# Kernel tuning notes

Hardware: AMD Instinct MI355X
Metric: run time of the kernel (lower is better)

Reference implementation:

```python
import jax, jax.numpy as jnp
import numpy as np

B, C, L, H = 4, 1024, 2048, 16
D = C // H


def setup_inputs() -> dict:
    key = jax.random.key(0)
    k1, k2, k3, k4 = jax.random.split(key, 4)
    queries = jax.random.normal(k1, (B, C, L), dtype=jnp.float32)
    mask = jax.random.randint(k2, (B, L), 0, 2, dtype=jnp.int32)
    # Conv1d(kernel_size=1, bias=False) weights, stored as [out_ch, in_ch]
    Wm = jax.random.normal(k3, (2 * C, C), dtype=jnp.float32) * (1.0 / np.sqrt(C))
    Wq = jax.random.normal(k4, (C, C), dtype=jnp.float32) * (1.0 / np.sqrt(C))
    return {"queries": queries, "mask": mask, "Wm": Wm, "Wq": Wq}


def reference(queries, mask, Wm, Wq):
    # 1x1 conv == channel-wise linear: [B,C,L] -> [B,L,out]
    mem = jnp.einsum("oc,bcl->blo", Wm, queries)   # [B, L, 2C]
    q = jnp.einsum("oc,bcl->blo", Wq, queries)      # [B, L, C]

    def split_heads(x):  # [B, L, C'] -> [B, H, L, D']
        b, l, c = x.shape
        return x.reshape(b, l, H, c // H).transpose(0, 2, 1, 3)

    Q = split_heads(q) * (D ** -0.5)                # [B, H, L, D]
    K = split_heads(mem[..., :C])                   # [B, H, L, D]
    V = split_heads(mem[..., C:])                   # [B, H, L, D]

    logits = jnp.einsum("bhqd,bhkd->bhqk", Q, K)    # [B, H, L, L]
    m = mask.astype(jnp.float32)[:, None, None, :]  # [B, 1, 1, L]
    NEG_INF = jnp.float32(-1e30)
    logits = logits * m + (1.0 - m) * NEG_INF
    weights = jax.nn.softmax(logits, axis=-1)
    x = jnp.einsum("bhqk,bhkd->bhqd", weights, V)   # [B, H, L, D]
    # combine heads and return [B, C, L]
    out = x.transpose(0, 2, 1, 3).reshape(B, L, C).transpose(0, 2, 1)
    return out
```

## Files before the change

kernel.cpp:

```cpp
#include <hip/hip_runtime.h>


typedef __bf16 bf16x8 __attribute__((ext_vector_type(8)));
typedef float f32x4 __attribute__((ext_vector_type(4)));
typedef float f32x16 __attribute__((ext_vector_type(16)));
typedef unsigned int u32x4 __attribute__((ext_vector_type(4)));

#define MFMA16(a, b, c) __builtin_amdgcn_mfma_f32_16x16x32_bf16((a), (b), (c), 0, 0, 0)
#define MFMA32(a, b, c) __builtin_amdgcn_mfma_f32_32x32x16_bf16((a), (b), (c), 0, 0, 0)

__device__ __forceinline__ unsigned short f2bf(float f) {
  unsigned int u = __float_as_uint(f);
  u += 0x7FFFu + ((u >> 16) & 1u);
  return (unsigned short)(u >> 16);
}

__device__ __forceinline__ void gload16(const void* g, void* lds) {
  __builtin_amdgcn_global_load_lds(
      (const __attribute__((address_space(1))) unsigned int*)g,
      (__attribute__((address_space(3))) unsigned int*)lds, 16, 0, 0);
}


__global__ __launch_bounds__(256) void castw_kernel(const float* __restrict__ Wm,
                                                    const float* __restrict__ Wq,
                                                    unsigned short* __restrict__ Wb) {
  size_t i = ((size_t)blockIdx.x * 256 + threadIdx.x) * 4;
  float4 v;
  if (i < (size_t)2048 * 1024) {
    v = *(const float4*)(Wm + i);
  } else {
    v = *(const float4*)(Wq + (i - (size_t)2048 * 1024));
    const float sc = 0.125f * 1.4426950408889634f;
    v.x *= sc; v.y *= sc; v.z *= sc; v.w *= sc;
  }
  ushort4 o;
  o.x = f2bf(v.x); o.y = f2bf(v.y); o.z = f2bf(v.z); o.w = f2bf(v.w);
  *(ushort4*)(Wb + i) = o;
}

__global__ __launch_bounds__(256) void transq_kernel(const float* __restrict__ q,
                                                     unsigned short* __restrict__ qT) {
  __shared__ float tile[32][33];
  int b = blockIdx.z;
  int l0 = blockIdx.x * 32, c0 = blockIdx.y * 32;
  int tx = threadIdx.x, ty = threadIdx.y;
  const float* src = q + ((size_t)b * 1024 + c0) * 2048 + l0;
#pragma unroll
  for (int i = 0; i < 4; i++)
    tile[ty + i * 8][tx] = src[(size_t)(ty + i * 8) * 2048 + tx];
  __syncthreads();
  unsigned short* dst = qT + ((size_t)b * 2048 + l0) * 1024 + c0;
#pragma unroll
  for (int i = 0; i < 4; i++)
    dst[(size_t)(ty + i * 8) * 1024 + tx] = f2bf(tile[tx][ty + i * 8]);
}

__global__ __launch_bounds__(256) void maskword_kernel(const int* __restrict__ mask,
                                                       unsigned int* __restrict__ mword) {
  int i = blockIdx.x * 256 + threadIdx.x;
  if (i < 4096) {
    const int* mp = mask + i * 2;
    mword[i] = (mp[0] ? 0xFFFFu : 0u) | (mp[1] ? 0xFFFF0000u : 0u);
  }
}


__global__ __launch_bounds__(256) void gemm_kernel(const unsigned short* __restrict__ Wb,
                                                   const unsigned short* __restrict__ qT,
                                                   unsigned short* __restrict__ Kb,
                                                   unsigned short* __restrict__ Vb,
                                                   unsigned short* __restrict__ Qb) {
  __shared__ __align__(16) unsigned short At[2][4096];
  __shared__ __align__(16) unsigned short Bt[2][4096];
  int n = blockIdx.x + 16 * (blockIdx.y + 24 * blockIdx.z);
  int lb = (n & 7) * 192 + (n >> 3);
  int bx = lb & 15;
  int by = (lb >> 4) % 24;
  int b = lb / 384;
  int o0 = by * 128, l0 = bx * 128;
  int tid = threadIdx.x, lane = tid & 63, wid = tid >> 6;
  int wr = wid >> 1, wc = wid & 1;
  int ln = lane & 15, g = lane >> 4;

  f32x4 acc[4][4];
#pragma unroll
  for (int m2 = 0; m2 < 4; m2++)
#pragma unroll
    for (int n2 = 0; n2 < 4; n2++) acc[m2][n2] = (f32x4){0.f, 0.f, 0.f, 0.f};

  const unsigned short* wsrc = Wb + (size_t)o0 * 1024;
  const unsigned short* xsrc = qT + ((size_t)b * 2048 + l0) * 1024;
  int c0 = tid, c1 = 256 + tid;

  {
    int kk = 0;
    gload16(wsrc + (size_t)(c0 >> 2) * 1024 + kk + (c0 & 3) * 8, (char*)At[0] + (size_t)wid * 1024);
    gload16(wsrc + (size_t)(c1 >> 2) * 1024 + kk + (c1 & 3) * 8, (char*)At[0] + 4096 + (size_t)wid * 1024);
    gload16(xsrc + (size_t)(c0 >> 2) * 1024 + kk + (c0 & 3) * 8, (char*)Bt[0] + (size_t)wid * 1024);
    gload16(xsrc + (size_t)(c1 >> 2) * 1024 + kk + (c1 & 3) * 8, (char*)Bt[0] + 4096 + (size_t)wid * 1024);
  }

  for (int t = 0; t < 32; t++) {
    int bs = t & 1;
    __builtin_amdgcn_sched_barrier(0);
    asm volatile("s_barrier" ::: "memory");
    if (t < 31) {
      int kk = (t + 1) * 32;
      gload16(wsrc + (size_t)(c0 >> 2) * 1024 + kk + (c0 & 3) * 8, (char*)At[bs ^ 1] + (size_t)wid * 1024);
      gload16(wsrc + (size_t)(c1 >> 2) * 1024 + kk + (c1 & 3) * 8, (char*)At[bs ^ 1] + 4096 + (size_t)wid * 1024);
      gload16(xsrc + (size_t)(c0 >> 2) * 1024 + kk + (c0 & 3) * 8, (char*)Bt[bs ^ 1] + (size_t)wid * 1024);
      gload16(xsrc + (size_t)(c1 >> 2) * 1024 + kk + (c1 & 3) * 8, (char*)Bt[bs ^ 1] + 4096 + (size_t)wid * 1024);
      asm volatile("s_waitcnt vmcnt(4)" ::: "memory");
    } else {
      asm volatile("s_waitcnt vmcnt(0)" ::: "memory");
    }
    asm volatile("s_barrier" ::: "memory");
    __builtin_amdgcn_sched_barrier(0);

    bf16x8 af[4], bfv[4];
#pragma unroll
    for (int m2 = 0; m2 < 4; m2++)
      af[m2] = *(const bf16x8*)&At[bs][(wr * 64 + m2 * 16 + ln) * 32 + g * 8];
#pragma unroll
    for (int n2 = 0; n2 < 4; n2++)
      bfv[n2] = *(const bf16x8*)&Bt[bs][(wc * 64 + n2 * 16 + ln) * 32 + g * 8];
    __builtin_amdgcn_s_setprio(1);
#pragma unroll
    for (int m2 = 0; m2 < 4; m2++)
#pragma unroll
      for (int n2 = 0; n2 < 4; n2++)
        acc[m2][n2] = MFMA16(af[m2], bfv[n2], acc[m2][n2]);
    __builtin_amdgcn_s_setprio(0);
  }

  int region = o0 >> 10;
#pragma unroll
  for (int m2 = 0; m2 < 4; m2++) {
    int orow = o0 + wr * 64 + m2 * 16 + g * 4;
#pragma unroll
    for (int n2 = 0; n2 < 4; n2++) {
      int l = l0 + wc * 64 + n2 * 16 + ln;
      if (region == 0) {
        int h = orow >> 6, d = orow & 63;
        ushort4 pk;
        pk.x = f2bf(acc[m2][n2][0]); pk.y = f2bf(acc[m2][n2][1]);
        pk.z = f2bf(acc[m2][n2][2]); pk.w = f2bf(acc[m2][n2][3]);
        *(ushort4*)&Kb[(((size_t)b * 16 + h) * 2048 + l) * 64 + d] = pk;
      } else if (region == 1) {
        int o2 = orow - 1024;
        int h = o2 >> 6, d = o2 & 63;
#pragma unroll
        for (int r = 0; r < 4; r++)
          Vb[(((size_t)b * 16 + h) * 64 + (d + r)) * 2048 + l] = f2bf(acc[m2][n2][r]);
      } else {
        int o2 = orow - 2048;
        int h = o2 >> 6, d = o2 & 63;
        ushort4 pk;
        pk.x = f2bf(acc[m2][n2][0]); pk.y = f2bf(acc[m2][n2][1]);
        pk.z = f2bf(acc[m2][n2][2]); pk.w = f2bf(acc[m2][n2][3]);
        *(ushort4*)&Qb[(((size_t)b * 16 + h) * 2048 + l) * 64 + d] = pk;
      }
    }
  }
}


__global__ __launch_bounds__(256) void attn_kernel(const unsigned short* __restrict__ Kb,
                                                   const unsigned short* __restrict__ Vb,
                                                   const unsigned short* __restrict__ Qb,
                                                   const unsigned int* __restrict__ mword,
                                                   float* __restrict__ out) {
  __shared__ __align__(16) unsigned short Kt[2][4096];
  __shared__ __align__(16) unsigned short Vt[2][4096];
  __shared__ __align__(16) unsigned int Mt[1024];

  int n = blockIdx.x;
  int lb = (n & 7) * 128 + (n >> 3);
  int qt = lb & 15;
  int bh = lb >> 4;
  int b = bh >> 4, h = bh & 15;
  int tid = threadIdx.x, lane = tid & 63, w = tid >> 6;
  int c = lane & 31, hi = lane >> 5;
  int q0 = qt * 128 + w * 32;

  const unsigned short* Kp = Kb + (size_t)bh * 2048 * 64;
  const unsigned short* Vp = Vb + (size_t)bh * 2048 * 64;
  const unsigned short* Qp = Qb + (size_t)bh * 2048 * 64;
  const unsigned int* mwp = mword + b * 1024;

  bf16x8 qf[4];
#pragma unroll
  for (int ks = 0; ks < 4; ks++)
    qf[ks] = *(const bf16x8*)&Qp[(size_t)(q0 + c) * 64 + ks * 16 + hi * 8];

  f32x16 fz;
#pragma unroll
  for (int i = 0; i < 16; i++) fz[i] = 0.f;
  f32x16 Ov0 = fz, Ov1 = fz, Os = fz;

  unsigned int ow = (c == 0) ? 0x3F803F80u : 0u;
  u32x4 ow4 = {ow, ow, ow, ow};
  bf16x8 bones = __builtin_bit_cast(bf16x8, ow4);

  int l8 = (lane & 7) * 16, l3 = lane >> 3;
  int cswz = (c & 7) << 4;

#pragma unroll
  for (int i = 0; i < 2; i++) {
    int widx = w * 2 + i;
    int row = widx * 8 + l3;
    int sb = l8 ^ ((row & 7) << 4);
    gload16((const char*)Kp + (size_t)row * 128 + sb, (char*)Kt[0] + widx * 1024);
    gload16((const char*)Vp + (size_t)row * 4096 + sb, (char*)Vt[0] + widx * 1024);
  }
  gload16((const char*)mwp + (size_t)w * 1024 + (size_t)lane * 16, (char*)Mt + w * 1024);

  for (int kb = 0; kb < 32; kb++) {
    int bs = kb & 1;
    __builtin_amdgcn_sched_barrier(0);
    asm volatile("s_barrier" ::: "memory");
    if (kb < 31) {
#pragma unroll
      for (int i = 0; i < 2; i++) {
        int widx = w * 2 + i;
        int row = widx * 8 + l3;
        int sb = l8 ^ ((row & 7) << 4);
        gload16((const char*)Kp + (size_t)(kb * 64 + 64 + row) * 128 + sb,
                (char*)Kt[bs ^ 1] + widx * 1024);
        gload16((const char*)Vp + (size_t)row * 4096 + (kb + 1) * 128 + sb,
                (char*)Vt[bs ^ 1] + widx * 1024);
      }
      asm volatile("s_waitcnt vmcnt(4)" ::: "memory");
    } else {
      asm volatile("s_waitcnt vmcnt(0)" ::: "memory");
    }
    asm volatile("s_barrier" ::: "memory");
    __builtin_amdgcn_sched_barrier(0);

    u32x4 mw[4];
#pragma unroll
    for (int ks2 = 0; ks2 < 4; ks2++)
      mw[ks2] = *(const u32x4*)((const char*)Mt + kb * 128 + ks2 * 32 + hi * 16);

    f32x16 s0, s1;
    const char* Kbuf = (const char*)Kt[bs];
    __builtin_amdgcn_s_setprio(1);
#pragma unroll
    for (int ks = 0; ks < 4; ks++) {
      int off = (ks * 32 + hi * 16) ^ cswz;
      bf16x8 a0 = *(const bf16x8*)(Kbuf + c * 128 + off);
      bf16x8 a1 = *(const bf16x8*)(Kbuf + (c + 32) * 128 + off);
      if (ks == 0) {
        s0 = MFMA32(a0, qf[0], fz);
        s1 = MFMA32(a1, qf[0], fz);
      } else {
        s0 = MFMA32(a0, qf[ks], s0);
        s1 = MFMA32(a1, qf[ks], s1);
      }
    }
    __builtin_amdgcn_s_setprio(0);
#pragma unroll
    for (int i = 0; i < 16; i++) {
      asm("v_exp_f32 %0, %1" : "=v"(s0[i]) : "v"(s0[i]));
      asm("v_exp_f32 %0, %1" : "=v"(s1[i]) : "v"(s1[i]));
    }
    bf16x8 pa[4];
#pragma unroll
    for (int ks2 = 0; ks2 < 4; ks2++) {
      int k1 = (ks2 & 1) * 8;
      unsigned int wds[4];
#pragma unroll
      for (int jj = 0; jj < 2; jj++) {
        unsigned int U, W;
        float u0 = (ks2 < 2) ? s0[k1 + 2 * jj] : s1[k1 + 2 * jj];
        float u1 = (ks2 < 2) ? s0[k1 + 2 * jj + 1] : s1[k1 + 2 * jj + 1];
        float w0 = (ks2 < 2) ? s0[k1 + 4 + 2 * jj] : s1[k1 + 4 + 2 * jj];
        float w1 = (ks2 < 2) ? s0[k1 + 5 + 2 * jj] : s1[k1 + 5 + 2 * jj];
        asm("v_cvt_pk_bf16_f32 %0, %1, %2" : "=v"(U) : "v"(u0), "v"(u1));
        asm("v_cvt_pk_bf16_f32 %0, %1, %2" : "=v"(W) : "v"(w0), "v"(w1));
        asm("v_permlane32_swap_b32 %0, %1" : "+v"(U), "+v"(W));
        wds[jj] = U;
        wds[2 + jj] = W;
      }
      u32x4 wv = {wds[0] & mw[ks2][0], wds[1] & mw[ks2][1],
                  wds[2] & mw[ks2][2], wds[3] & mw[ks2][3]};
      pa[ks2] = __builtin_bit_cast(bf16x8, wv);
    }
    const char* Vbuf = (const char*)Vt[bs];
    __builtin_amdgcn_s_setprio(1);
#pragma unroll
    for (int ks2 = 0; ks2 < 4; ks2++) {
      int off = (ks2 * 32 + hi * 16) ^ cswz;
      bf16x8 v0 = *(const bf16x8*)(Vbuf + c * 128 + off);
      bf16x8 v1 = *(const bf16x8*)(Vbuf + (c + 32) * 128 + off);
      Ov0 = MFMA32(pa[ks2], v0, Ov0);
      Ov1 = MFMA32(pa[ks2], v1, Ov1);
      Os = MFMA32(pa[ks2], bones, Os);
    }
    __builtin_amdgcn_s_setprio(0);
  }

  float rinv[16];
#pragma unroll
  for (int r = 0; r < 16; r++) {
    float d0 = __int_as_float(__builtin_amdgcn_readlane(__float_as_int(Os[r]), 0));
    float d1 = __int_as_float(__builtin_amdgcn_readlane(__float_as_int(Os[r]), 32));
    rinv[r] = __builtin_amdgcn_rcpf(hi ? d1 : d0);
  }

  size_t obase = ((size_t)b * 1024 + h * 64) * 2048 + q0;
#pragma unroll
  for (int g2 = 0; g2 < 4; g2++) {
    int lq = g2 * 8 + hi * 4;
    float4 x0, x1;
    x0.x = Ov0[g2 * 4 + 0] * rinv[g2 * 4 + 0]; x0.y = Ov0[g2 * 4 + 1] * rinv[g2 * 4 + 1];
    x0.z = Ov0[g2 * 4 + 2] * rinv[g2 * 4 + 2]; x0.w = Ov0[g2 * 4 + 3] * rinv[g2 * 4 + 3];
    x1.x = Ov1[g2 * 4 + 0] * rinv[g2 * 4 + 0]; x1.y = Ov1[g2 * 4 + 1] * rinv[g2 * 4 + 1];
    x1.z = Ov1[g2 * 4 + 2] * rinv[g2 * 4 + 2]; x1.w = Ov1[g2 * 4 + 3] * rinv[g2 * 4 + 3];
    *(float4*)(out + obase + (size_t)c * 2048 + lq) = x0;
    *(float4*)(out + obase + (size_t)(32 + c) * 2048 + lq) = x1;
  }
}

extern "C" void kernel_launch(void* const* d_in, const int* in_sizes, int n_in,
                              void* d_out, int out_size, void* d_ws, size_t ws_size,
                              hipStream_t stream) {
  const float* queries = (const float*)d_in[0];
  const int* mask = (const int*)d_in[1];
  const float* Wm = (const float*)d_in[2];
  const float* Wq = (const float*)d_in[3];
  float* out = (float*)d_out;

  char* ws = (char*)d_ws;
  unsigned short* Wb = (unsigned short*)(ws);
  unsigned short* qT = (unsigned short*)(ws + 6291456);
  unsigned short* Kb = (unsigned short*)(ws + 23068672);
  unsigned short* Vb = (unsigned short*)(ws + 39845888);
  unsigned short* Qb = (unsigned short*)(ws + 56623104);
  unsigned int* mwp = (unsigned int*)(ws + 73400320);

  castw_kernel<<<3072, 256, 0, stream>>>(Wm, Wq, Wb);
  transq_kernel<<<dim3(64, 32, 4), dim3(32, 8), 0, stream>>>(queries, qT);
  maskword_kernel<<<16, 256, 0, stream>>>(mask, mwp);
  gemm_kernel<<<dim3(16, 24, 4), 256, 0, stream>>>(Wb, qT, Kb, Vb, Qb);
  attn_kernel<<<1024, 256, 0, stream>>>(Kb, Vb, Qb, mwp, out);
}
```

Before: 266.3 us.

## Load V fragments directly from global into registers instead of via LDS

Drops the V double buffer in shared memory. Each wave now reads its V MFMA operands straight from global memory (V stored d-major) as bf16x8 vectors, issued early in each iteration and waited on with hand-tuned vmcnt counts. This removes LDS traffic and LDS footprint for V, which could allow higher occupancy. In exchange every wave redundantly fetches the same V tile from global/L2, and the manual vmcnt accounting is fragile.

```diff
diff --git a/kernel.cpp b/kernel.cpp
--- a/kernel.cpp
+++ b/kernel.cpp
@@ -172,7 +172,6 @@
                                                    const unsigned int* __restrict__ mword,
                                                    float* __restrict__ out) {
   __shared__ __align__(16) unsigned short Kt[2][4096];
-  __shared__ __align__(16) unsigned short Vt[2][4096];
   __shared__ __align__(16) unsigned int Mt[1024];
 
   int n = blockIdx.x;
@@ -212,14 +211,19 @@
     int row = widx * 8 + l3;
     int sb = l8 ^ ((row & 7) << 4);
     gload16((const char*)Kp + (size_t)row * 128 + sb, (char*)Kt[0] + widx * 1024);
-    gload16((const char*)Vp + (size_t)row * 4096 + sb, (char*)Vt[0] + widx * 1024);
   }
   gload16((const char*)mwp + (size_t)w * 1024 + (size_t)lane * 16, (char*)Mt + w * 1024);
+
+#define VLOAD(d_, ks_) \
+  (*(const bf16x8*)&Vp[(size_t)(d_)*2048 + kb * 64 + (ks_)*16 + hi * 8])
 
   for (int kb = 0; kb < 32; kb++) {
     int bs = kb & 1;
     __builtin_amdgcn_sched_barrier(0);
     asm volatile("s_barrier" ::: "memory");
+
+    bf16x8 v00 = VLOAD(c, 0), v01 = VLOAD(c + 32, 0);
+    bf16x8 v10 = VLOAD(c, 1), v11 = VLOAD(c + 32, 1);
     if (kb < 31) {
 #pragma unroll
       for (int i = 0; i < 2; i++) {
@@ -228,13 +232,9 @@
         int sb = l8 ^ ((row & 7) << 4);
         gload16((const char*)Kp + (size_t)(kb * 64 + 64 + row) * 128 + sb,
                 (char*)Kt[bs ^ 1] + widx * 1024);
-        gload16((const char*)Vp + (size_t)row * 4096 + (kb + 1) * 128 + sb,
-                (char*)Vt[bs ^ 1] + widx * 1024);
       }
-      asm volatile("s_waitcnt vmcnt(4)" ::: "memory");
-    } else {
-      asm volatile("s_waitcnt vmcnt(0)" ::: "memory");
-    }
+    }
+    asm volatile("s_waitcnt vmcnt(6)" ::: "memory");
     asm volatile("s_barrier" ::: "memory");
     __builtin_amdgcn_sched_barrier(0);
 
@@ -287,19 +287,34 @@
                   wds[2] & mw[ks2][2], wds[3] & mw[ks2][3]};
       pa[ks2] = __builtin_bit_cast(bf16x8, wv);
     }
-    const char* Vbuf = (const char*)Vt[bs];
+
+    bf16x8 v20 = VLOAD(c, 2), v21 = VLOAD(c + 32, 2);
+    bf16x8 v30 = VLOAD(c, 3), v31 = VLOAD(c + 32, 3);
+
+    if (kb < 31) {
+      asm volatile("s_waitcnt vmcnt(6)" ::: "memory");
+    } else {
+      asm volatile("s_waitcnt vmcnt(4)" ::: "memory");
+    }
     __builtin_amdgcn_s_setprio(1);
-#pragma unroll
-    for (int ks2 = 0; ks2 < 4; ks2++) {
-      int off = (ks2 * 32 + hi * 16) ^ cswz;
-      bf16x8 v0 = *(const bf16x8*)(Vbuf + c * 128 + off);
-      bf16x8 v1 = *(const bf16x8*)(Vbuf + (c + 32) * 128 + off);
-      Ov0 = MFMA32(pa[ks2], v0, Ov0);
-      Ov1 = MFMA32(pa[ks2], v1, Ov1);
-      Os = MFMA32(pa[ks2], bones, Os);
-    }
+    Ov0 = MFMA32(pa[0], v00, Ov0);
+    Ov1 = MFMA32(pa[0], v01, Ov1);
+    Os = MFMA32(pa[0], bones, Os);
+    Ov0 = MFMA32(pa[1], v10, Ov0);
+    Ov1 = MFMA32(pa[1], v11, Ov1);
+    Os = MFMA32(pa[1], bones, Os);
     __builtin_amdgcn_s_setprio(0);
-  }
+    asm volatile("s_waitcnt vmcnt(0)" ::: "memory");
+    __builtin_amdgcn_s_setprio(1);
+    Ov0 = MFMA32(pa[2], v20, Ov0);
+    Ov1 = MFMA32(pa[2], v21, Ov1);
+    Os = MFMA32(pa[2], bones, Os);
+    Ov0 = MFMA32(pa[3], v30, Ov0);
+    Ov1 = MFMA32(pa[3], v31, Ov1);
+    Os = MFMA32(pa[3], bones, Os);
+    __builtin_amdgcn_s_setprio(0);
+  }
+#undef VLOAD
 
   float rinv[16];
 #pragma unroll
```

After: 291.2 us. +9.4%, slower.
